# Optimization experiments

Measured on AMD Instinct MI355X. Metric: run time of the kernel, lower is better.

## Reference

```python
import jax, jax.numpy as jnp
import numpy as np

N_NODES = 100000
N_EDGES = 1600000
N_FEAT = 128
HIDDEN = 64
NUM_GRAPHS = 64


def setup_inputs() -> dict:
    key = jax.random.key(0)
    ks = jax.random.split(key, 10)
    x = jax.random.normal(ks[0], (N_NODES, N_FEAT), dtype=jnp.float32)
    W = jax.random.normal(ks[1], (N_FEAT, HIDDEN), dtype=jnp.float32) * (1.0 / np.sqrt(N_FEAT))
    b = jax.random.normal(ks[2], (HIDDEN,), dtype=jnp.float32) * 0.01
    W1 = jax.random.normal(ks[3], (HIDDEN, 16), dtype=jnp.float32) * (1.0 / np.sqrt(HIDDEN))
    b1 = jax.random.normal(ks[4], (16,), dtype=jnp.float32) * 0.01
    W2 = jax.random.normal(ks[5], (16, 1), dtype=jnp.float32) * 0.25
    b2 = jax.random.normal(ks[6], (1,), dtype=jnp.float32) * 0.01
    edge_index = jax.random.randint(ks[7], (2, N_EDGES), 0, N_NODES, dtype=jnp.int64)
    batch = jnp.sort(jax.random.randint(ks[8], (N_NODES,), 0, NUM_GRAPHS, dtype=jnp.int64))
    return {"x": x, "W": W, "b": b, "W1": W1, "b1": b1, "W2": W2, "b2": b2,
            "edge_index": edge_index, "batch": batch, "num_graphs": NUM_GRAPHS}


def reference(x, W, b, W1, b1, W2, b2, edge_index, batch, num_graphs):
    N = x.shape[0]
    # GCNConv: h = D^-1/2 (A + I) D^-1/2 (x W) + b
    h = x @ W  # [N, H]
    loops = jnp.arange(N, dtype=edge_index.dtype)
    src = jnp.concatenate([edge_index[0], loops])  # source nodes (with self-loops)
    dst = jnp.concatenate([edge_index[1], loops])  # target nodes
    deg = jax.ops.segment_sum(jnp.ones(dst.shape, h.dtype), dst, num_segments=N)
    dis = jnp.where(deg > 0, jax.lax.rsqrt(deg), 0.0)  # deg^-1/2, 0 for isolated
    norm = dis[src] * dis[dst]  # [E+N]
    msg = h[src] * norm[:, None]  # gather + normalize
    agg = jax.ops.segment_sum(msg, dst, num_segments=N) + b  # scatter-add + bias
    hn = jax.nn.relu(agg)
    # global_add_pool over graphs
    u = jax.ops.segment_sum(hn, batch, num_segments=num_graphs)  # [G, H]
    out = jax.nn.relu(u @ W1 + b1) @ W2 + b2  # [G, 1]
    return out.reshape(-1)
```

## Files before the change

kernel.cpp:

```cpp
#include <hip/hip_runtime.h>

#define N_NODES   100000
#define N_FEAT    128
#define N_EDGES   1600000
#define HIDDEN    64
#define NUM_GRAPHS 64
#define CHUNK   8192
#define NCHUNK  ((N_EDGES + CHUNK - 1) / CHUNK)
#define BSHIFT  8
#define NBUCKET ((N_NODES + 255) >> 8)
#define OFFS_W  (NBUCKET + 1)

typedef unsigned int  uint32;
typedef unsigned short ushort16;

typedef __attribute__((ext_vector_type(8))) __bf16 bf16x8;
typedef __attribute__((ext_vector_type(4))) float  f32x4;
union Frag8 { bf16x8 v; unsigned short s[8]; uint4 q; };

static __device__ __forceinline__ unsigned short f2bf(float f) {
    uint32 u = __float_as_uint(f);
    u += 0x7fffu + ((u >> 16) & 1u);
    return (unsigned short)(u >> 16);
}

__global__ __launch_bounds__(256) void w_transpose(const float* __restrict__ W,
                                                   ushort16* __restrict__ Wt) {
    const int base = blockIdx.x * 1024 + threadIdx.x;
#pragma unroll
    for (int j = 0; j < 4; ++j) {
        const int idx = base + j * 256;
        const int k = idx >> 6, n = idx & 63;
        Wt[n * N_FEAT + k] = f2bf(W[idx]);
    }
}

__global__ __launch_bounds__(256) void gemm_xw(const float* __restrict__ x,
                                               const ushort16* __restrict__ Wt,
                                               ushort16* __restrict__ hb) {
    const int lane = threadIdx.x & 63;
    const int wv   = threadIdx.x >> 6;
    const int m15  = lane & 15;
    const int quad = lane >> 4;
    const int base = blockIdx.x * 64 + wv * 16;
    const int arow = min(base + m15, N_NODES - 1);

    const float* xr = &x[(size_t)arow * N_FEAT + quad * 8];
    float4 xa[4][2];
#pragma unroll
    for (int kc = 0; kc < 4; ++kc) {
        xa[kc][0] = *(const float4*)&xr[kc * 32];
        xa[kc][1] = *(const float4*)&xr[kc * 32 + 4];
    }

    Frag8 bf[4][4];
#pragma unroll
    for (int nt = 0; nt < 4; ++nt) {
        const ushort16* wr = &Wt[(nt * 16 + m15) * N_FEAT + quad * 8];
#pragma unroll
        for (int kc = 0; kc < 4; ++kc)
            bf[nt][kc].q = *(const uint4*)&wr[kc * 32];
    }

    Frag8 af[4];
#pragma unroll
    for (int kc = 0; kc < 4; ++kc) {
        const float* f = (const float*)&xa[kc][0];
#pragma unroll
        for (int j = 0; j < 8; ++j) af[kc].s[j] = f2bf(f[j]);
    }

    f32x4 acc[4];
#pragma unroll
    for (int nt = 0; nt < 4; ++nt) acc[nt] = (f32x4){0.f, 0.f, 0.f, 0.f};

#pragma unroll
    for (int kc = 0; kc < 4; ++kc)
#pragma unroll
        for (int nt = 0; nt < 4; ++nt)
            acc[nt] = __builtin_amdgcn_mfma_f32_16x16x32_bf16(af[kc].v, bf[nt][kc].v,
                                                              acc[nt], 0, 0, 0);

#pragma unroll
    for (int r = 0; r < 4; ++r) {
        const int orow = base + quad * 4 + r;
        if (orow < N_NODES) {
#pragma unroll
            for (int nt = 0; nt < 4; ++nt)
                hb[(size_t)orow * HIDDEN + nt * 16 + m15] = f2bf(acc[nt][r]);
        }
    }
}

__global__ __launch_bounds__(512) void partition_kernel(const int* __restrict__ ei,
                                                        int* __restrict__ src_out,
                                                        unsigned char* __restrict__ dst8,
                                                        int* __restrict__ offs,
                                                        int* __restrict__ bucket_size) {
    __shared__ int hist[512];
    __shared__ int excl[512];
    __shared__ int ssrc[CHUNK];
    __shared__ int sdst[CHUNK];
    const int c = blockIdx.x;
    const int base = c * CHUNK;
    const int n = min(CHUNK, N_EDGES - base);
    const int t = threadIdx.x;
    hist[t] = 0;
    __syncthreads();

    int es[CHUNK / 512], ed[CHUNK / 512], rk[CHUNK / 512];
#pragma unroll
    for (int k = 0; k < CHUNK / 512; ++k) {
        const int i = t + k * 512;
        if (i < n) {
            ed[k] = __builtin_nontemporal_load(&ei[N_EDGES + base + i]);
            es[k] = __builtin_nontemporal_load(&ei[base + i]);
            rk[k] = atomicAdd(&hist[ed[k] >> BSHIFT], 1);
        }
    }
    __syncthreads();

    const int cnt = hist[t];
    for (int off = 1; off < 512; off <<= 1) {
        const int v = (t >= off) ? hist[t - off] : 0;
        __syncthreads();
        hist[t] += v;
        __syncthreads();
    }
    excl[t] = hist[t] - cnt;
    __syncthreads();
    if (t <= NBUCKET) offs[c * OFFS_W + t] = base + excl[t];
    if (t < NBUCKET && cnt > 0) atomicAdd(&bucket_size[t], cnt);

#pragma unroll
    for (int k = 0; k < CHUNK / 512; ++k) {
        const int i = t + k * 512;
        if (i < n) {
            const int pos = excl[ed[k] >> BSHIFT] + rk[k];
            ssrc[pos] = es[k];
            sdst[pos] = ed[k];
        }
    }
    __syncthreads();

    for (int i = t; i < n; i += 512)
        src_out[base + i] = ssrc[i];
    for (int i = t * 4; i < n; i += 2048) {
        const uint32 p = (uint32)(sdst[i] & 255)
                       | ((uint32)(sdst[i + 1] & 255) << 8)
                       | ((uint32)(sdst[i + 2] & 255) << 16)
                       | ((uint32)(sdst[i + 3] & 255) << 24);
        *(uint32*)&dst8[base + i] = p;
    }
}

__global__ __launch_bounds__(512) void scan_buckets(const int* __restrict__ bucket_size,
                                                    int* __restrict__ bucket_start) {
    __shared__ int s[512];
    const int t = threadIdx.x;
    const int v = (t < NBUCKET) ? bucket_size[t] : 0;
    s[t] = v;
    __syncthreads();
    for (int off = 1; off < 512; off <<= 1) {
        const int a = (t >= off) ? s[t - off] : 0;
        __syncthreads();
        s[t] += a;
        __syncthreads();
    }
    if (t < NBUCKET) bucket_start[t] = s[t] - v;
}

__global__ __launch_bounds__(512) void bucket_csr(const int* __restrict__ offs,
                                                  const int* __restrict__ src_tmp,
                                                  const unsigned char* __restrict__ dst8,
                                                  const int* __restrict__ bucket_start,
                                                  int* __restrict__ srcs,
                                                  int* __restrict__ row_ptr,
                                                  int* __restrict__ row_end,
                                                  float* __restrict__ dis) {
    __shared__ int hist[256];
    __shared__ int nxt[256];
    __shared__ int segb[NCHUNK], sege[NCHUNK];
    const int b = blockIdx.x;
    const int lo = b << BSHIFT;
    const int t = threadIdx.x;
    const int lane = t & 63;
    const int wv = t >> 6;
    const int bstart = bucket_start[b];

    if (t < 256) hist[t] = 0;
    for (int c = t; c < NCHUNK; c += 512) {
        segb[c] = offs[c * OFFS_W + b];
        sege[c] = offs[c * OFFS_W + b + 1];
    }
    __syncthreads();

    for (int c = wv; c < NCHUNK; c += 8)
        for (int i = segb[c] + lane; i < sege[c]; i += 64)
            atomicAdd(&hist[dst8[i]], 1);
    __syncthreads();

    const int cnt = (t < 256) ? hist[t] : 0;
    for (int off = 1; off < 256; off <<= 1) {
        int v = 0;
        if (t < 256 && t >= off) v = hist[t - off];
        __syncthreads();
        if (t < 256) hist[t] += v;
        __syncthreads();
    }
    if (t < 256) {
        const int excl = hist[t] - cnt;
        nxt[t] = excl;
        const int node = lo + t;
        if (node < N_NODES) {
            row_ptr[node] = bstart + excl;
            row_end[node] = bstart + excl + cnt;
            dis[node]     = rsqrtf((float)cnt + 1.0f);
        }
    }
    __syncthreads();

    for (int c = wv; c < NCHUNK; c += 8)
        for (int i = segb[c] + lane; i < sege[c]; i += 64) {
            const int d = dst8[i];
            const int s = src_tmp[i];
            const int pos = atomicAdd(&nxt[d], 1);
            srcs[bstart + pos] = s;
        }
}

__global__ __launch_bounds__(256) void agg_kernel(const int* __restrict__ row_ptr,
                                                  const int* __restrict__ row_end,
                                                  const int* __restrict__ srcs,
                                                  const ushort16* __restrict__ hb,
                                                  const float* __restrict__ dis,
                                                  const float* __restrict__ bias,
                                                  const int* __restrict__ batch,
                                                  float* __restrict__ u) {
    __shared__ float sp[32][HIDDEN + 1];
    __shared__ int gbs[32];
    const int t = threadIdx.x;
    const int lane = t & 63;
    const int wv = t >> 6;
    const int g = lane >> 3;
    const int k = lane & 7;
    const int kb = lane & 56;
    const int base = blockIdx.x * 32;
    const int node = base + wv * 8 + g;
    const int beg = row_ptr[node];
    const int end = row_end[node];
    const int deg = end - beg;
    const float dn = dis[node];

    int dmax = deg;
    dmax = max(dmax, __shfl_xor(dmax, 8));
    dmax = max(dmax, __shfl_xor(dmax, 16));
    dmax = max(dmax, __shfl_xor(dmax, 32));

    float acc[8];
#pragma unroll
    for (int j = 0; j < 8; ++j) acc[j] = 0.f;

    for (int i0 = 0; i0 < dmax; i0 += 8) {
        int idx = beg + i0 + k;
        idx = min(idx, end - 1);
        idx = max(idx, 0);
        const int s8 = srcs[idx];
        const float w8 = dis[s8] * dn;

        int   si[8];
        float wi[8];
#pragma unroll
        for (int j = 0; j < 8; ++j) {
            si[j] = __shfl(s8, kb | j);
            const float w = __shfl(w8, kb | j);
            wi[j] = (i0 + j < deg) ? w : 0.f;
        }
        uint4 v[8];
#pragma unroll
        for (int j = 0; j < 8; ++j)
            v[j] = *(const uint4*)&hb[(size_t)si[j] * HIDDEN + k * 8];
#pragma unroll
        for (int j = 0; j < 8; ++j) {
            acc[0] = fmaf(__uint_as_float(v[j].x << 16),         wi[j], acc[0]);
            acc[1] = fmaf(__uint_as_float(v[j].x & 0xffff0000u), wi[j], acc[1]);
            acc[2] = fmaf(__uint_as_float(v[j].y << 16),         wi[j], acc[2]);
            acc[3] = fmaf(__uint_as_float(v[j].y & 0xffff0000u), wi[j], acc[3]);
            acc[4] = fmaf(__uint_as_float(v[j].z << 16),         wi[j], acc[4]);
            acc[5] = fmaf(__uint_as_float(v[j].z & 0xffff0000u), wi[j], acc[5]);
            acc[6] = fmaf(__uint_as_float(v[j].w << 16),         wi[j], acc[6]);
            acc[7] = fmaf(__uint_as_float(v[j].w & 0xffff0000u), wi[j], acc[7]);
        }
    }

    {
        const uint4 hv = *(const uint4*)&hb[(size_t)node * HIDDEN + k * 8];
        const float d2 = dn * dn;
        const float4 b0 = *(const float4*)&bias[k * 8];
        const float4 b1 = *(const float4*)&bias[k * 8 + 4];
        float4 r0, r1;
        r0.x = fmaxf(fmaf(__uint_as_float(hv.x << 16),         d2, acc[0]) + b0.x, 0.f);
        r0.y = fmaxf(fmaf(__uint_as_float(hv.x & 0xffff0000u), d2, acc[1]) + b0.y, 0.f);
        r0.z = fmaxf(fmaf(__uint_as_float(hv.y << 16),         d2, acc[2]) + b0.z, 0.f);
        r0.w = fmaxf(fmaf(__uint_as_float(hv.y & 0xffff0000u), d2, acc[3]) + b0.w, 0.f);
        r1.x = fmaxf(fmaf(__uint_as_float(hv.z << 16),         d2, acc[4]) + b1.x, 0.f);
        r1.y = fmaxf(fmaf(__uint_as_float(hv.z & 0xffff0000u), d2, acc[5]) + b1.y, 0.f);
        r1.z = fmaxf(fmaf(__uint_as_float(hv.w << 16),         d2, acc[6]) + b1.z, 0.f);
        r1.w = fmaxf(fmaf(__uint_as_float(hv.w & 0xffff0000u), d2, acc[7]) + b1.w, 0.f);
        *(float4*)&sp[wv * 8 + g][k * 8]     = r0;
        *(float4*)&sp[wv * 8 + g][k * 8 + 4] = r1;
    }
    if (t < 32) gbs[t] = batch[base + t];
    __syncthreads();

    if (t < 64) {
        float a = sp[0][t];
        int cg = gbs[0];
        for (int r = 1; r < 32; ++r) {
            const int gr = gbs[r];
            const float vv = sp[r][t];
            if (gr == cg) a += vv;
            else { atomicAdd(&u[cg * HIDDEN + t], a); cg = gr; a = vv; }
        }
        atomicAdd(&u[cg * HIDDEN + t], a);
    }
}

__global__ __launch_bounds__(64) void mlp_kernel(const float* __restrict__ u,
                                                 const float* __restrict__ W1,
                                                 const float* __restrict__ b1,
                                                 const float* __restrict__ W2,
                                                 const float* __restrict__ b2,
                                                 float* __restrict__ out) {
    __shared__ float W1s[HIDDEN * 16];
    __shared__ float W2s[16];
    __shared__ float b1s[16];
    const int t = threadIdx.x;
    for (int i = t; i < HIDDEN * 16; i += 64) W1s[i] = W1[i];
    if (t < 16) { W2s[t] = W2[t]; b1s[t] = b1[t]; }
    __syncthreads();
    if (t < NUM_GRAPHS) {
        float uu[HIDDEN];
#pragma unroll
        for (int k = 0; k < HIDDEN; ++k) uu[k] = u[t * HIDDEN + k];
        float o = b2[0];
#pragma unroll
        for (int j = 0; j < 16; ++j) {
            float s = b1s[j];
#pragma unroll
            for (int k = 0; k < HIDDEN; ++k) s = fmaf(uu[k], W1s[k * 16 + j], s);
            o = fmaf(fmaxf(s, 0.f), W2s[j], o);
        }
        out[t] = o;
    }
}

extern "C" void kernel_launch(void* const* d_in, const int* in_sizes, int n_in,
                              void* d_out, int out_size, void* d_ws, size_t ws_size,
                              hipStream_t stream) {
    const float* x  = (const float*)d_in[0];
    const float* W  = (const float*)d_in[1];
    const float* b  = (const float*)d_in[2];
    const float* W1 = (const float*)d_in[3];
    const float* b1 = (const float*)d_in[4];
    const float* W2 = (const float*)d_in[5];
    const float* b2 = (const float*)d_in[6];
    const int*   ei = (const int*)d_in[7];
    const int* batch = (const int*)d_in[8];
    float* out = (float*)d_out;

    ushort16* hb       = (ushort16*)d_ws;
    int*      src_tmp  = (int*)(hb + (size_t)N_NODES * HIDDEN);
    unsigned char* dst8 = (unsigned char*)(src_tmp + N_EDGES);
    int*      srcs     = (int*)(dst8 + N_EDGES);
    int*      offs     = srcs + N_EDGES;
    int*      row_ptr  = offs + NCHUNK * OFFS_W;
    int*      row_end  = row_ptr + N_NODES;
    float*    dis      = (float*)(row_end + N_NODES);
    int*      bucket_size  = (int*)(dis + N_NODES);
    int*      bucket_start = bucket_size + 512;
    float*    u        = (float*)(bucket_start + 512);
    ushort16* Wtg      = (ushort16*)(u + NUM_GRAPHS * HIDDEN);

    hipMemsetAsync(bucket_size, 0, 512 * sizeof(int), stream);
    hipMemsetAsync(u, 0, NUM_GRAPHS * HIDDEN * sizeof(float), stream);

    w_transpose<<<8, 256, 0, stream>>>(W, Wtg);
    gemm_xw<<<(N_NODES + 63) / 64, 256, 0, stream>>>(x, Wtg, hb);
    partition_kernel<<<NCHUNK, 512, 0, stream>>>(ei, src_tmp, dst8, offs, bucket_size);
    scan_buckets<<<1, 512, 0, stream>>>(bucket_size, bucket_start);
    bucket_csr<<<NBUCKET, 512, 0, stream>>>(offs, src_tmp, dst8, bucket_start,
                                            srcs, row_ptr, row_end, dis);
    agg_kernel<<<N_NODES / 32, 256, 0, stream>>>(row_ptr, row_end, srcs, hb, dis, b, batch, u);
    mlp_kernel<<<1, 64, 0, stream>>>(u, W1, b1, W2, b2, out);
}
```

Before: 205.8 us.

## Drop bucket scan kernel and stage bucket CSR scatter in shared memory

```diff
diff --git a/kernel.cpp b/kernel.cpp
--- a/kernel.cpp
+++ b/kernel.cpp
@@ -10,6 +10,7 @@
 #define BSHIFT  8
 #define NBUCKET ((N_NODES + 255) >> 8)
 #define OFFS_W  (NBUCKET + 1)
+#define CAP     4800
 
 typedef unsigned int  uint32;
 typedef unsigned short ushort16;
@@ -95,8 +96,7 @@
 __global__ __launch_bounds__(512) void partition_kernel(const int* __restrict__ ei,
                                                         int* __restrict__ src_out,
                                                         unsigned char* __restrict__ dst8,
-                                                        int* __restrict__ offs,
-                                                        int* __restrict__ bucket_size) {
+                                                        int* __restrict__ offs) {
     __shared__ int hist[512];
     __shared__ int excl[512];
     __shared__ int ssrc[CHUNK];
@@ -130,7 +130,6 @@
     excl[t] = hist[t] - cnt;
     __syncthreads();
     if (t <= NBUCKET) offs[c * OFFS_W + t] = base + excl[t];
-    if (t < NBUCKET && cnt > 0) atomicAdd(&bucket_size[t], cnt);
 
 #pragma unroll
     for (int k = 0; k < CHUNK / 512; ++k) {
@@ -154,50 +153,73 @@
     }
 }
 
-__global__ __launch_bounds__(512) void scan_buckets(const int* __restrict__ bucket_size,
-                                                    int* __restrict__ bucket_start) {
-    __shared__ int s[512];
-    const int t = threadIdx.x;
-    const int v = (t < NBUCKET) ? bucket_size[t] : 0;
-    s[t] = v;
-    __syncthreads();
-    for (int off = 1; off < 512; off <<= 1) {
-        const int a = (t >= off) ? s[t - off] : 0;
-        __syncthreads();
-        s[t] += a;
-        __syncthreads();
-    }
-    if (t < NBUCKET) bucket_start[t] = s[t] - v;
-}
-
 __global__ __launch_bounds__(512) void bucket_csr(const int* __restrict__ offs,
                                                   const int* __restrict__ src_tmp,
                                                   const unsigned char* __restrict__ dst8,
-                                                  const int* __restrict__ bucket_start,
                                                   int* __restrict__ srcs,
                                                   int* __restrict__ row_ptr,
                                                   int* __restrict__ row_end,
                                                   float* __restrict__ dis) {
     __shared__ int hist[256];
     __shared__ int nxt[256];
-    __shared__ int segb[NCHUNK], sege[NCHUNK];
+    __shared__ int segb[NCHUNK];
+    __shared__ int pre[NCHUNK + 1];
+    __shared__ int sc[256];
+    __shared__ int ssrc[CAP];
+    __shared__ int sb;
     const int b = blockIdx.x;
     const int lo = b << BSHIFT;
     const int t = threadIdx.x;
-    const int lane = t & 63;
-    const int wv = t >> 6;
-    const int bstart = bucket_start[b];
 
     if (t < 256) hist[t] = 0;
-    for (int c = t; c < NCHUNK; c += 512) {
-        segb[c] = offs[c * OFFS_W + b];
-        sege[c] = offs[c * OFFS_W + b + 1];
-    }
-    __syncthreads();
-
-    for (int c = wv; c < NCHUNK; c += 8)
-        for (int i = segb[c] + lane; i < sege[c]; i += 64)
-            atomicAdd(&hist[dst8[i]], 1);
+    if (t == 0) sb = 0;
+    __syncthreads();
+
+    int len = 0;
+    if (t < NCHUNK) {
+        const int s0 = offs[t * OFFS_W + b];
+        const int s1 = offs[t * OFFS_W + b + 1];
+        segb[t] = s0;
+        len = s1 - s0;
+        atomicAdd(&sb, s0 - t * CHUNK);
+    }
+    if (t < 256) sc[t] = (t < NCHUNK) ? len : 0;
+    __syncthreads();
+    for (int off = 1; off < 256; off <<= 1) {
+        int v = 0;
+        if (t < 256 && t >= off) v = sc[t - off];
+        __syncthreads();
+        if (t < 256) sc[t] += v;
+        __syncthreads();
+    }
+    if (t == 0) pre[0] = 0;
+    if (t < NCHUNK) pre[t + 1] = sc[t];
+    __syncthreads();
+
+    const int total  = pre[NCHUNK];
+    const int bstart = sb;
+    const bool fits  = (total <= CAP);
+
+    int es[(CAP + 511) / 512], ed[(CAP + 511) / 512], rk[(CAP + 511) / 512];
+    int ne = 0;
+    if (fits) {
+        for (int e = t; e < total; e += 512) {
+            int l2 = 0, h2 = NCHUNK;
+            while (h2 - l2 > 1) { const int mid = (l2 + h2) >> 1;
+                                  if (pre[mid] <= e) l2 = mid; else h2 = mid; }
+            const int gidx = segb[l2] + (e - pre[l2]);
+            const int d = dst8[gidx];
+            const int s = src_tmp[gidx];
+            es[ne] = s; ed[ne] = d;
+            rk[ne] = atomicAdd(&hist[d], 1);
+            ++ne;
+        }
+    } else {
+        const int lane = t & 63, wv = t >> 6;
+        for (int c = wv; c < NCHUNK; c += 8)
+            for (int i = segb[c] + lane; i < segb[c] + (pre[c + 1] - pre[c]); i += 64)
+                atomicAdd(&hist[dst8[i]], 1);
+    }
     __syncthreads();
 
     const int cnt = (t < 256) ? hist[t] : 0;
@@ -220,13 +242,21 @@
     }
     __syncthreads();
 
-    for (int c = wv; c < NCHUNK; c += 8)
-        for (int i = segb[c] + lane; i < sege[c]; i += 64) {
-            const int d = dst8[i];
-            const int s = src_tmp[i];
-            const int pos = atomicAdd(&nxt[d], 1);
-            srcs[bstart + pos] = s;
-        }
+    if (fits) {
+        for (int k = 0; k < ne; ++k)
+            ssrc[nxt[ed[k]] + rk[k]] = es[k];
+        __syncthreads();
+        for (int i = t; i < total; i += 512)
+            srcs[bstart + i] = ssrc[i];
+    } else {
+        const int lane = t & 63, wv = t >> 6;
+        for (int c = wv; c < NCHUNK; c += 8)
+            for (int i = segb[c] + lane; i < segb[c] + (pre[c + 1] - pre[c]); i += 64) {
+                const int d = dst8[i];
+                const int pos = atomicAdd(&nxt[d], 1);
+                srcs[bstart + pos] = src_tmp[i];
+            }
+    }
 }
 
 __global__ __launch_bounds__(256) void agg_kernel(const int* __restrict__ row_ptr,
@@ -377,19 +407,15 @@
     int*      row_ptr  = offs + NCHUNK * OFFS_W;
     int*      row_end  = row_ptr + N_NODES;
     float*    dis      = (float*)(row_end + N_NODES);
-    int*      bucket_size  = (int*)(dis + N_NODES);
-    int*      bucket_start = bucket_size + 512;
-    float*    u        = (float*)(bucket_start + 512);
+    float*    u        = dis + N_NODES;
     ushort16* Wtg      = (ushort16*)(u + NUM_GRAPHS * HIDDEN);
 
-    hipMemsetAsync(bucket_size, 0, 512 * sizeof(int), stream);
     hipMemsetAsync(u, 0, NUM_GRAPHS * HIDDEN * sizeof(float), stream);
 
     w_transpose<<<8, 256, 0, stream>>>(W, Wtg);
     gemm_xw<<<(N_NODES + 63) / 64, 256, 0, stream>>>(x, Wtg, hb);
-    partition_kernel<<<NCHUNK, 512, 0, stream>>>(ei, src_tmp, dst8, offs, bucket_size);
-    scan_buckets<<<1, 512, 0, stream>>>(bucket_size, bucket_start);
-    bucket_csr<<<NBUCKET, 512, 0, stream>>>(offs, src_tmp, dst8, bucket_start,
+    partition_kernel<<<NCHUNK, 512, 0, stream>>>(ei, src_tmp, dst8, offs);
+    bucket_csr<<<NBUCKET, 512, 0, stream>>>(offs, src_tmp, dst8,
                                             srcs, row_ptr, row_end, dis);
     agg_kernel<<<N_NODES / 32, 256, 0, stream>>>(row_ptr, row_end, srcs, hb, dis, b, batch, u);
     mlp_kernel<<<1, 64, 0, stream>>>(u, W1, b1, W2, b2, out);
```

Result: faster. 188.8 us (-8.3%).
